# Performance work log

Hardware: AMD Instinct MI355X
Metric: run time of the kernel (lower is better)

## Reference

```python
import jax, jax.numpy as jnp
import numpy as np

N_DIALOGS = 60
DIA_LEN = 100
N = N_DIALOGS * DIA_LEN  # 6000 utterances total
D_IN = 512
D_OUT = 512


def setup_inputs() -> dict:
    key = jax.random.key(0)
    k1, k2, k3, k4 = jax.random.split(key, 4)
    inputs = jax.random.normal(k1, (N, D_IN), dtype=jnp.float32)
    # per-dialog lengths (concrete host array; defines static graph structure)
    dia_len = np.full((N_DIALOGS,), DIA_LEN, dtype=np.int64)
    # one-hot speaker mask [N, 1, 2]; qmask[j,0,0]==1 -> speaker0 else speaker1
    sp = jax.random.randint(k2, (N,), 0, 2)
    qmask = jnp.zeros((N, 1, 2), jnp.int64).at[jnp.arange(N), 0, sp].set(1)
    W = jax.random.normal(k3, (D_OUT, D_IN), dtype=jnp.float32) / np.sqrt(D_IN)
    b = jax.random.normal(k4, (D_OUT,), dtype=jnp.float32) * 0.01
    return {"inputs": inputs, "dia_len": dia_len, "qmask": qmask, "W": W, "b": b}


def build_adj(inputs, dia_len, qmask):
    # Vectorized equivalent of message_passing_directed_speaker:
    # adj = I; edge (i,j) iff i,j in same dialog, same speaker, and consecutive
    # among that speaker's utterances; weight = 1 - arccos(clip(cos,-1,1))/pi.
    n = inputs.shape[0]
    dia_len_np = np.asarray(dia_len)
    did = jnp.asarray(np.repeat(np.arange(len(dia_len_np)), dia_len_np))  # dialog id per node
    sp0 = qmask[:, 0, 0] == 1  # True -> speaker0
    cs0 = jnp.cumsum(sp0.astype(jnp.int32))
    cs1 = jnp.cumsum((~sp0).astype(jnp.int32))
    csel = jnp.where(sp0, cs0, cs1)  # running count of own speaker
    idx = jnp.arange(n)
    # j>i, same dialog, same speaker, no same-speaker utterance strictly between
    upper = ((did[None, :] == did[:, None])
             & (sp0[None, :] == sp0[:, None])
             & (csel[None, :] - csel[:, None] == 1)
             & (idx[None, :] > idx[:, None]))
    edge = upper | upper.T
    # pairwise cosine similarity (cossim returns 0 when a norm is 0)
    nrm = jnp.sqrt(jnp.sum(inputs * inputs, axis=-1))  # [N]
    denom = nrm[:, None] * nrm[None, :]
    dots = inputs @ inputs.T  # [N, N]
    cos = jnp.where(denom > 0, dots / jnp.where(denom > 0, denom, 1.0), 0.0)
    cos_safe = jnp.where(edge, jnp.clip(cos, -1.0, 1.0), 0.0)
    w = 1.0 - jnp.arccos(cos_safe) / jnp.pi
    return jnp.where(edge, w, 0.0) + jnp.eye(n, dtype=inputs.dtype)


def reference(inputs, dia_len, qmask, W, b):
    adj = build_adj(inputs, dia_len, qmask)  # [N, N]
    x = adj @ inputs                          # [N, D_IN]
    return x @ W.T + b                        # [N, D_OUT]
```

## Files before the change

kernel.cpp:

```cpp
#include <hip/hip_runtime.h>
#include <hip/hip_bf16.h>

#define N_NODES 6000
#define N_DIA   60
#define DIA     100
#define DDIM    512
#define NPAD    6016

typedef short short8   __attribute__((ext_vector_type(8)));
typedef float floatx4  __attribute__((ext_vector_type(4)));

__device__ __forceinline__ unsigned short f2bf(float f) {
    unsigned int u = __float_as_uint(f);
    unsigned int r = (u + 0x7fffu + ((u >> 16) & 1u)) >> 16;
    return (unsigned short)r;
}

__device__ __forceinline__ float wave_reduce_sum(float v) {
    #pragma unroll
    for (int off = 32; off > 0; off >>= 1) v += __shfl_xor(v, off, 64);
    return v;
}

__global__ __launch_bounds__(1024) void fused_prep(
    const float* __restrict__ x, const int* __restrict__ qmask,
    const float* __restrict__ W, unsigned short* __restrict__ xbf,
    unsigned short* __restrict__ wbf)
{
    int bid = blockIdx.x;
    int tid = threadIdx.x;
    if (bid >= N_DIA) {
        int base = (bid - N_DIA) * 8192 + tid * 8;
        float4 a = *(const float4*)(W + base);
        float4 b = *(const float4*)(W + base + 4);
        union { unsigned short u[8]; short8 v; } o;
        o.u[0]=f2bf(a.x); o.u[1]=f2bf(a.y); o.u[2]=f2bf(a.z); o.u[3]=f2bf(a.w);
        o.u[4]=f2bf(b.x); o.u[5]=f2bf(b.y); o.u[6]=f2bf(b.z); o.u[7]=f2bf(b.w);
        *(short8*)(wbf + base) = o.v;
        if (bid == N_DIA) {
            short8 z = (short8)0;
            *(short8*)(xbf + (size_t)N_NODES * DDIM + tid * 8) = z;
        }
        return;
    }

    __shared__ float nrm2_s[DIA];
    __shared__ float wn_s[DIA];
    __shared__ int   sp_s[DIA];
    __shared__ int   nxt_s[DIA];
    __shared__ int   prv_s[DIA];

    int nbase = bid * DIA;
    int wv = tid >> 6, lane = tid & 63;

    if (tid < DIA) sp_s[tid] = qmask[2 * (nbase + tid)];
    __syncthreads();

    if (tid < DIA) {
        int sp = sp_s[tid];
        int nx = -1;
        for (int j = tid + 1; j < DIA; ++j) if (sp_s[j] == sp) { nx = j; break; }
        int pv = -1;
        for (int j = tid - 1; j >= 0; --j) if (sp_s[j] == sp) { pv = j; break; }
        nxt_s[tid] = nx; prv_s[tid] = pv;
    }

    for (int r = wv; r < DIA; r += 16) {
        const float* row = x + (size_t)(nbase + r) * DDIM + lane * 8;
        float4 a = *(const float4*)(row);
        float4 b = *(const float4*)(row + 4);
        float s = a.x*a.x + a.y*a.y + a.z*a.z + a.w*a.w
                + b.x*b.x + b.y*b.y + b.z*b.z + b.w*b.w;
        s = wave_reduce_sum(s);
        if (lane == 0) nrm2_s[r] = s;
    }
    __syncthreads();

    for (int r = wv; r < DIA; r += 16) {
        int j = nxt_s[r];
        if (j >= 0) {
            const float* ri = x + (size_t)(nbase + r) * DDIM + lane * 8;
            const float* rj = x + (size_t)(nbase + j) * DDIM + lane * 8;
            float4 a0 = *(const float4*)(ri);
            float4 a1 = *(const float4*)(ri + 4);
            float4 b0 = *(const float4*)(rj);
            float4 b1 = *(const float4*)(rj + 4);
            float d = a0.x*b0.x + a0.y*b0.y + a0.z*b0.z + a0.w*b0.w
                    + a1.x*b1.x + a1.y*b1.y + a1.z*b1.z + a1.w*b1.w;
            d = wave_reduce_sum(d);
            if (lane == 0) {
                float dn = nrm2_s[r] * nrm2_s[j];
                float c = (dn > 0.0f) ? (d / sqrtf(dn)) : 0.0f;
                c = fminf(1.0f, fmaxf(-1.0f, c));
                wn_s[r] = 1.0f - acosf(c) * 0.3183098861837907f;
            }
        } else if (lane == 0) {
            wn_s[r] = 0.0f;
        }
    }
    __syncthreads();

    for (int r = wv; r < DIA; r += 16) {
        const float* ri = x + (size_t)(nbase + r) * DDIM + lane * 8;
        float acc[8];
        {
            float4 a = *(const float4*)(ri);
            float4 b = *(const float4*)(ri + 4);
            acc[0]=a.x; acc[1]=a.y; acc[2]=a.z; acc[3]=a.w;
            acc[4]=b.x; acc[5]=b.y; acc[6]=b.z; acc[7]=b.w;
        }
        int j = nxt_s[r];
        if (j >= 0) {
            float w = wn_s[r];
            const float* rj = x + (size_t)(nbase + j) * DDIM + lane * 8;
            float4 a = *(const float4*)(rj);
            float4 b = *(const float4*)(rj + 4);
            acc[0]+=w*a.x; acc[1]+=w*a.y; acc[2]+=w*a.z; acc[3]+=w*a.w;
            acc[4]+=w*b.x; acc[5]+=w*b.y; acc[6]+=w*b.z; acc[7]+=w*b.w;
        }
        int p = prv_s[r];
        if (p >= 0) {
            float w = wn_s[p];
            const float* rp = x + (size_t)(nbase + p) * DDIM + lane * 8;
            float4 a = *(const float4*)(rp);
            float4 b = *(const float4*)(rp + 4);
            acc[0]+=w*a.x; acc[1]+=w*a.y; acc[2]+=w*a.z; acc[3]+=w*a.w;
            acc[4]+=w*b.x; acc[5]+=w*b.y; acc[6]+=w*b.z; acc[7]+=w*b.w;
        }
        union { unsigned short u[8]; short8 v; } o;
        #pragma unroll
        for (int t = 0; t < 8; ++t) o.u[t] = f2bf(acc[t]);
        *(short8*)(xbf + (size_t)(nbase + r) * DDIM + lane * 8) = o.v;
    }
}

__global__ __launch_bounds__(256) void gemm_kernel(
    const unsigned short* __restrict__ xbf, const unsigned short* __restrict__ wbf,
    const float* __restrict__ bias, float* __restrict__ out)
{
    int wave = threadIdx.x >> 6, lane = threadIdx.x & 63;
    int m0 = blockIdx.x * 64 + (wave & 1) * 32;
    int n0 = blockIdx.y * 64 + (wave >> 1) * 32;
    int fr = lane & 15;
    int kq = (lane >> 4) * 8;

    floatx4 acc[2][2] = {};
    const unsigned short* ab = xbf + (size_t)(m0 + fr) * DDIM + kq;
    const unsigned short* bb = wbf + (size_t)(n0 + fr) * DDIM + kq;

    #pragma unroll 4
    for (int k = 0; k < DDIM; k += 32) {
        short8 a0 = *(const short8*)(ab + k);
        short8 a1 = *(const short8*)(ab + 16 * DDIM + k);
        short8 b0 = *(const short8*)(bb + k);
        short8 b1 = *(const short8*)(bb + 16 * DDIM + k);
        acc[0][0] = __builtin_amdgcn_mfma_f32_16x16x32_bf16(a0, b0, acc[0][0], 0, 0, 0);
        acc[0][1] = __builtin_amdgcn_mfma_f32_16x16x32_bf16(a0, b1, acc[0][1], 0, 0, 0);
        acc[1][0] = __builtin_amdgcn_mfma_f32_16x16x32_bf16(a1, b0, acc[1][0], 0, 0, 0);
        acc[1][1] = __builtin_amdgcn_mfma_f32_16x16x32_bf16(a1, b1, acc[1][1], 0, 0, 0);
    }

    int col = lane & 15;
    int rbase = (lane >> 4) * 4;
    #pragma unroll
    for (int ms = 0; ms < 2; ++ms) {
        #pragma unroll
        for (int ns = 0; ns < 2; ++ns) {
            int n = n0 + ns * 16 + col;
            float bv = bias[n];
            #pragma unroll
            for (int r = 0; r < 4; ++r) {
                int m = m0 + ms * 16 + rbase + r;
                if (m < N_NODES)
                    out[(size_t)m * DDIM + n] = acc[ms][ns][r] + bv;
            }
        }
    }
}

extern "C" void kernel_launch(void* const* d_in, const int* in_sizes, int n_in,
                              void* d_out, int out_size, void* d_ws, size_t ws_size,
                              hipStream_t stream) {
    const float* inputs = (const float*)d_in[0];
    const int* qmask   = (const int*)d_in[2];
    const float* W     = (const float*)d_in[3];
    const float* bias  = (const float*)d_in[4];
    float* out = (float*)d_out;

    char* ws = (char*)d_ws;
    unsigned short* xbf = (unsigned short*)ws;
    unsigned short* wbf = xbf + (size_t)NPAD * DDIM;

    fused_prep <<<dim3(N_DIA + 32), 1024, 0, stream>>>(inputs, qmask, W, xbf, wbf);
    gemm_kernel<<<dim3(94, 8),      256,  0, stream>>>(xbf, wbf, bias, out);
}
```

Before: 111.2 us.

## Parallelize edge computation per node and fuse neighbor aggregation into GEMM

Graph-edge detection and cosine weights now run one wave per node, using ballot-based search for the next and previous same-speaker utterance. This replaces 60 large blocks that each did a serial per-dialog scan. Neighbor aggregation moves into the GEMM kernel, which builds a 64-row bf16 tile in LDS and multiplies it by all 512 output columns, so the bf16 intermediate no longer makes a global round trip. The trade-off is that the GEMM now launches only 94 blocks, so fewer CUs do the matrix work.

```diff
diff --git a/kernel.cpp b/kernel.cpp
--- a/kernel.cpp
+++ b/kernel.cpp
@@ -5,7 +5,7 @@
 #define N_DIA   60
 #define DIA     100
 #define DDIM    512
-#define NPAD    6016
+#define LDA     520
 
 typedef short short8   __attribute__((ext_vector_type(8)));
 typedef float floatx4  __attribute__((ext_vector_type(4)));
@@ -22,86 +22,98 @@
     return v;
 }
 
-__global__ __launch_bounds__(1024) void fused_prep(
+__global__ __launch_bounds__(256) void edge_kernel(
     const float* __restrict__ x, const int* __restrict__ qmask,
-    const float* __restrict__ W, unsigned short* __restrict__ xbf,
-    unsigned short* __restrict__ wbf)
+    const float* __restrict__ W, int* __restrict__ nxt, int* __restrict__ prv,
+    float* __restrict__ wn, unsigned short* __restrict__ wbf)
 {
     int bid = blockIdx.x;
     int tid = threadIdx.x;
-    if (bid >= N_DIA) {
-        int base = (bid - N_DIA) * 8192 + tid * 8;
+    if (bid >= N_NODES / 4) {
+        int base = (bid - N_NODES / 4) * 2048 + tid * 8;
         float4 a = *(const float4*)(W + base);
         float4 b = *(const float4*)(W + base + 4);
         union { unsigned short u[8]; short8 v; } o;
         o.u[0]=f2bf(a.x); o.u[1]=f2bf(a.y); o.u[2]=f2bf(a.z); o.u[3]=f2bf(a.w);
         o.u[4]=f2bf(b.x); o.u[5]=f2bf(b.y); o.u[6]=f2bf(b.z); o.u[7]=f2bf(b.w);
         *(short8*)(wbf + base) = o.v;
-        if (bid == N_DIA) {
-            short8 z = (short8)0;
-            *(short8*)(xbf + (size_t)N_NODES * DDIM + tid * 8) = z;
-        }
         return;
     }
-
-    __shared__ float nrm2_s[DIA];
-    __shared__ float wn_s[DIA];
-    __shared__ int   sp_s[DIA];
-    __shared__ int   nxt_s[DIA];
-    __shared__ int   prv_s[DIA];
-
-    int nbase = bid * DIA;
     int wv = tid >> 6, lane = tid & 63;
-
-    if (tid < DIA) sp_s[tid] = qmask[2 * (nbase + tid)];
-    __syncthreads();
-
-    if (tid < DIA) {
-        int sp = sp_s[tid];
-        int nx = -1;
-        for (int j = tid + 1; j < DIA; ++j) if (sp_s[j] == sp) { nx = j; break; }
-        int pv = -1;
-        for (int j = tid - 1; j >= 0; --j) if (sp_s[j] == sp) { pv = j; break; }
-        nxt_s[tid] = nx; prv_s[tid] = pv;
-    }
-
-    for (int r = wv; r < DIA; r += 16) {
-        const float* row = x + (size_t)(nbase + r) * DDIM + lane * 8;
-        float4 a = *(const float4*)(row);
-        float4 b = *(const float4*)(row + 4);
-        float s = a.x*a.x + a.y*a.y + a.z*a.z + a.w*a.w
-                + b.x*b.x + b.y*b.y + b.z*b.z + b.w*b.w;
-        s = wave_reduce_sum(s);
-        if (lane == 0) nrm2_s[r] = s;
-    }
-    __syncthreads();
-
-    for (int r = wv; r < DIA; r += 16) {
-        int j = nxt_s[r];
-        if (j >= 0) {
-            const float* ri = x + (size_t)(nbase + r) * DDIM + lane * 8;
-            const float* rj = x + (size_t)(nbase + j) * DDIM + lane * 8;
-            float4 a0 = *(const float4*)(ri);
-            float4 a1 = *(const float4*)(ri + 4);
-            float4 b0 = *(const float4*)(rj);
-            float4 b1 = *(const float4*)(rj + 4);
-            float d = a0.x*b0.x + a0.y*b0.y + a0.z*b0.z + a0.w*b0.w
-                    + a1.x*b1.x + a1.y*b1.y + a1.z*b1.z + a1.w*b1.w;
-            d = wave_reduce_sum(d);
-            if (lane == 0) {
-                float dn = nrm2_s[r] * nrm2_s[j];
-                float c = (dn > 0.0f) ? (d / sqrtf(dn)) : 0.0f;
-                c = fminf(1.0f, fmaxf(-1.0f, c));
-                wn_s[r] = 1.0f - acosf(c) * 0.3183098861837907f;
-            }
-        } else if (lane == 0) {
-            wn_s[r] = 0.0f;
-        }
-    }
-    __syncthreads();
-
-    for (int r = wv; r < DIA; r += 16) {
-        const float* ri = x + (size_t)(nbase + r) * DDIM + lane * 8;
+    int i = bid * 4 + wv;
+    int sp = qmask[2 * i];
+    int dstart = (i / DIA) * DIA;
+    int dend   = dstart + DIA;
+
+    int cand = i + 1 + lane;
+    unsigned long long b1 = __ballot(cand < dend && qmask[2 * cand] == sp);
+    int j = -1;
+    if (b1) j = i + __ffsll(b1);
+    else {
+        int c2 = i + 65 + lane;
+        unsigned long long b2 = __ballot(lane < 35 && c2 < dend && qmask[2 * c2] == sp);
+        if (b2) j = i + 64 + __ffsll(b2);
+    }
+    int candp = i - 1 - lane;
+    unsigned long long p1 = __ballot(candp >= dstart && qmask[2 * candp] == sp);
+    int p = -1;
+    if (p1) p = i - __ffsll(p1);
+    else {
+        int pc2 = i - 65 - lane;
+        unsigned long long p2 = __ballot(lane < 35 && pc2 >= dstart && qmask[2 * pc2] == sp);
+        if (p2) p = i - 64 - __ffsll(p2);
+    }
+
+    float w = 0.0f;
+    if (j >= 0) {
+        const float* ri = x + (size_t)i * DDIM + lane * 8;
+        const float* rj = x + (size_t)j * DDIM + lane * 8;
+        float4 a0 = *(const float4*)(ri);
+        float4 a1 = *(const float4*)(ri + 4);
+        float4 b0 = *(const float4*)(rj);
+        float4 b1 = *(const float4*)(rj + 4);
+        float d  = a0.x*b0.x + a0.y*b0.y + a0.z*b0.z + a0.w*b0.w
+                 + a1.x*b1.x + a1.y*b1.y + a1.z*b1.z + a1.w*b1.w;
+        float ni = a0.x*a0.x + a0.y*a0.y + a0.z*a0.z + a0.w*a0.w
+                 + a1.x*a1.x + a1.y*a1.y + a1.z*a1.z + a1.w*a1.w;
+        float nj = b0.x*b0.x + b0.y*b0.y + b0.z*b0.z + b0.w*b0.w
+                 + b1.x*b1.x + b1.y*b1.y + b1.z*b1.z + b1.w*b1.w;
+        d  = wave_reduce_sum(d);
+        ni = wave_reduce_sum(ni);
+        nj = wave_reduce_sum(nj);
+        float dn = ni * nj;
+        float c = (dn > 0.0f) ? (d * __frsqrt_rn(dn)) : 0.0f;
+        c = fminf(1.0f, fmaxf(-1.0f, c));
+        w = 1.0f - acosf(c) * 0.3183098861837907f;
+    }
+    if (lane == 0) { nxt[i] = j; prv[i] = p; wn[i] = w; }
+}
+
+__global__ __launch_bounds__(512) void build_gemm(
+    const float* __restrict__ x, const int* __restrict__ nxt,
+    const int* __restrict__ prv, const float* __restrict__ wn,
+    const unsigned short* __restrict__ wbf, const float* __restrict__ bias,
+    float* __restrict__ out)
+{
+    __shared__ unsigned short As[64 * LDA];
+    int tid = threadIdx.x;
+    int wv = tid >> 6, lane = tid & 63;
+    int m0 = blockIdx.x * 64;
+
+    #pragma unroll 2
+    for (int t = 0; t < 8; ++t) {
+        int rr = wv * 8 + t;
+        int i = m0 + rr;
+        unsigned short* dst = As + rr * LDA + lane * 8;
+        if (i >= N_NODES) {
+            *(short8*)dst = (short8)0;
+            continue;
+        }
+        int j = nxt[i];
+        int p = prv[i];
+        float wi = (j >= 0) ? wn[i] : 0.0f;
+        float wp = (p >= 0) ? wn[p] : 0.0f;
+        const float* ri = x + (size_t)i * DDIM + lane * 8;
         float acc[8];
         {
             float4 a = *(const float4*)(ri);
@@ -109,63 +121,57 @@
             acc[0]=a.x; acc[1]=a.y; acc[2]=a.z; acc[3]=a.w;
             acc[4]=b.x; acc[5]=b.y; acc[6]=b.z; acc[7]=b.w;
         }
-        int j = nxt_s[r];
         if (j >= 0) {
-            float w = wn_s[r];
-            const float* rj = x + (size_t)(nbase + j) * DDIM + lane * 8;
+            const float* rj = x + (size_t)j * DDIM + lane * 8;
             float4 a = *(const float4*)(rj);
             float4 b = *(const float4*)(rj + 4);
-            acc[0]+=w*a.x; acc[1]+=w*a.y; acc[2]+=w*a.z; acc[3]+=w*a.w;
-            acc[4]+=w*b.x; acc[5]+=w*b.y; acc[6]+=w*b.z; acc[7]+=w*b.w;
-        }
-        int p = prv_s[r];
+            acc[0]+=wi*a.x; acc[1]+=wi*a.y; acc[2]+=wi*a.z; acc[3]+=wi*a.w;
+            acc[4]+=wi*b.x; acc[5]+=wi*b.y; acc[6]+=wi*b.z; acc[7]+=wi*b.w;
+        }
         if (p >= 0) {
-            float w = wn_s[p];
-            const float* rp = x + (size_t)(nbase + p) * DDIM + lane * 8;
+            const float* rp = x + (size_t)p * DDIM + lane * 8;
             float4 a = *(const float4*)(rp);
             float4 b = *(const float4*)(rp + 4);
-            acc[0]+=w*a.x; acc[1]+=w*a.y; acc[2]+=w*a.z; acc[3]+=w*a.w;
-            acc[4]+=w*b.x; acc[5]+=w*b.y; acc[6]+=w*b.z; acc[7]+=w*b.w;
+            acc[0]+=wp*a.x; acc[1]+=wp*a.y; acc[2]+=wp*a.z; acc[3]+=wp*a.w;
+            acc[4]+=wp*b.x; acc[5]+=wp*b.y; acc[6]+=wp*b.z; acc[7]+=wp*b.w;
         }
         union { unsigned short u[8]; short8 v; } o;
         #pragma unroll
-        for (int t = 0; t < 8; ++t) o.u[t] = f2bf(acc[t]);
-        *(short8*)(xbf + (size_t)(nbase + r) * DDIM + lane * 8) = o.v;
-    }
-}
-
-__global__ __launch_bounds__(256) void gemm_kernel(
-    const unsigned short* __restrict__ xbf, const unsigned short* __restrict__ wbf,
-    const float* __restrict__ bias, float* __restrict__ out)
-{
-    int wave = threadIdx.x >> 6, lane = threadIdx.x & 63;
-    int m0 = blockIdx.x * 64 + (wave & 1) * 32;
-    int n0 = blockIdx.y * 64 + (wave >> 1) * 32;
+        for (int q = 0; q < 8; ++q) o.u[q] = f2bf(acc[q]);
+        *(short8*)dst = o.v;
+    }
+    __syncthreads();
+
+    int n0 = wv * 64;
     int fr = lane & 15;
     int kq = (lane >> 4) * 8;
-
-    floatx4 acc[2][2] = {};
-    const unsigned short* ab = xbf + (size_t)(m0 + fr) * DDIM + kq;
+    floatx4 acc[4][4] = {};
+    const unsigned short* As_base = As + fr * LDA + kq;
     const unsigned short* bb = wbf + (size_t)(n0 + fr) * DDIM + kq;
 
-    #pragma unroll 4
+    #pragma unroll 2
     for (int k = 0; k < DDIM; k += 32) {
-        short8 a0 = *(const short8*)(ab + k);
-        short8 a1 = *(const short8*)(ab + 16 * DDIM + k);
-        short8 b0 = *(const short8*)(bb + k);
-        short8 b1 = *(const short8*)(bb + 16 * DDIM + k);
-        acc[0][0] = __builtin_amdgcn_mfma_f32_16x16x32_bf16(a0, b0, acc[0][0], 0, 0, 0);
-        acc[0][1] = __builtin_amdgcn_mfma_f32_16x16x32_bf16(a0, b1, acc[0][1], 0, 0, 0);
-        acc[1][0] = __builtin_amdgcn_mfma_f32_16x16x32_bf16(a1, b0, acc[1][0], 0, 0, 0);
-        acc[1][1] = __builtin_amdgcn_mfma_f32_16x16x32_bf16(a1, b1, acc[1][1], 0, 0, 0);
+        short8 af[4], bfv[4];
+        #pragma unroll
+        for (int ms = 0; ms < 4; ++ms)
+            af[ms] = *(const short8*)(As_base + ms * 16 * LDA + k);
+        #pragma unroll
+        for (int ns = 0; ns < 4; ++ns)
+            bfv[ns] = *(const short8*)(bb + (size_t)ns * 16 * DDIM + k);
+        #pragma unroll
+        for (int ms = 0; ms < 4; ++ms)
+            #pragma unroll
+            for (int ns = 0; ns < 4; ++ns)
+                acc[ms][ns] = __builtin_amdgcn_mfma_f32_16x16x32_bf16(
+                    af[ms], bfv[ns], acc[ms][ns], 0, 0, 0);
     }
 
     int col = lane & 15;
     int rbase = (lane >> 4) * 4;
     #pragma unroll
-    for (int ms = 0; ms < 2; ++ms) {
-        #pragma unroll
-        for (int ns = 0; ns < 2; ++ns) {
+    for (int ms = 0; ms < 4; ++ms) {
+        #pragma unroll
+        for (int ns = 0; ns < 4; ++ns) {
             int n = n0 + ns * 16 + col;
             float bv = bias[n];
             #pragma unroll
@@ -188,9 +194,13 @@
     float* out = (float*)d_out;
 
     char* ws = (char*)d_ws;
-    unsigned short* xbf = (unsigned short*)ws;
-    unsigned short* wbf = xbf + (size_t)NPAD * DDIM;
-
-    fused_prep <<<dim3(N_DIA + 32), 1024, 0, stream>>>(inputs, qmask, W, xbf, wbf);
-    gemm_kernel<<<dim3(94, 8),      256,  0, stream>>>(xbf, wbf, bias, out);
-}
+    unsigned short* wbf = (unsigned short*)ws;
+    float* wn  = (float*)(ws + 524288);
+    int*   nxt = (int*)(ws + 524288 + 24576);
+    int*   prv = (int*)(ws + 524288 + 2 * 24576);
+
+    edge_kernel<<<dim3(N_NODES / 4 + 128), 256, 0, stream>>>(
+        inputs, qmask, W, nxt, prv, wn, wbf);
+    build_gemm <<<dim3(94),               512, 0, stream>>>(
+        inputs, nxt, prv, wn, wbf, bias, out);
+}
```

New measurement: 99.83 us. 1.11x faster.
